# Kernel tuning notes

Hardware: AMD Instinct MI355X
Metric: run time of the kernel (lower is better)

## Reference

```python
import jax, jax.numpy as jnp
import numpy as np

H, N, CH = 256, 64, 1

def _r2c(x):
    return x[..., 0] + 1j * x[..., 1]

def setup_inputs() -> dict:
    key = jax.random.key(0)
    kA, kB, kC, kdt = jax.random.split(key, 4)
    # Build a Hurwitz A (skew-Hermitian - 0.5*I) so dA = (I-dt/2 A)^-1 (I+dt/2 A) has spectral radius < 1
    M = jax.random.normal(kA, (H, N, N, 2), dtype=jnp.float32) / np.float32(np.sqrt(N))
    Mc = _r2c(M)
    Ac = 0.5 * (Mc - jnp.conjugate(jnp.swapaxes(Mc, -1, -2))) - 0.5 * jnp.eye(N, dtype=Mc.dtype)
    A = jnp.stack([Ac.real, Ac.imag], axis=-1)  # (H,N,N,2)
    B = jax.random.normal(kB, (H, N, 2), dtype=jnp.float32)
    C = jax.random.normal(kC, (CH, H, N, 2), dtype=jnp.float32)
    # log_dt uniform in [log(1e-3), log(1e-1)], shape (H,1) per bilinear docstring
    log_dt = jax.random.uniform(kdt, (H, 1), dtype=jnp.float32,
                                minval=np.float32(np.log(1e-3)), maxval=np.float32(np.log(1e-1)))
    return {"A": A, "B": B, "C": C, "log_dt": log_dt, "L": 2048}

def _bilinear(dt, Ac, Bc):
    # dt: (H,1), Ac: (H,N,N) complex, Bc: (H,N) complex
    n = Ac.shape[-1]
    I = jnp.eye(n, dtype=Ac.dtype)
    half = (dt.astype(Ac.real.dtype) / 2)[:, None]  # (H,1,1)
    A_back = I - half * Ac
    A_fwd = I + half * Ac
    dB = dt.astype(Ac.dtype) * jnp.linalg.solve(A_back, Bc[..., None])[..., 0]  # (H,N)
    dA = jnp.linalg.solve(A_back, A_fwd)  # (H,N,N)
    return dA, dB

def _krylov(L, dA, dB):
    # x[..., l] = dA^l dB via squaring-doubling, matches S4 krylov math
    x = dB[..., None]  # (H,N,1)
    A_ = dA
    while x.shape[-1] < L:
        x = jnp.concatenate([x, jnp.einsum('hnm,hml->hnl', A_, x)], axis=-1)
        A_ = A_ @ A_
    return x[..., :L]

def reference(A, B, C, log_dt, L):
    Ac, Bc, Cc = _r2c(A), _r2c(B), _r2c(C)
    dt = jnp.exp(log_dt)  # (H,1)
    dA, dB = _bilinear(dt, Ac, Bc)
    x = _krylov(L, dA, dB)  # (H,N,L) complex
    # k[c,h,l] = sum_n C[c,h,n] * (dA^l dB)[h,n]; torch .float() on complex keeps real part
    k = jnp.einsum('chn,hnl->chl', Cc, x).real.astype(jnp.float32)
    return k
```

## Files before the change

kernel.cpp:

```cpp
#include <hip/hip_runtime.h>
#include <math.h>

#define NH   256
#define NN   64
#define LSEQ 2048
#define RSW  68
#define NTH  1024

typedef __attribute__((ext_vector_type(8))) short short8;
typedef __attribute__((ext_vector_type(4))) float float4_t;
typedef __attribute__((ext_vector_type(16))) float float16_t;
typedef unsigned short u16;

#define MFMA(a,b,c)   __builtin_amdgcn_mfma_f32_16x16x32_bf16((a),(b),(c),0,0,0)
#define MFMA32(a,b,c) __builtin_amdgcn_mfma_f32_32x32x16_bf16((a),(b),(c),0,0,0)
#define PERM_HI 0x07060302u
#define PERM_LO 0x05040100u

static __device__ __forceinline__ void split2(float v, unsigned& hb, unsigned& lb) {
    hb = __float_as_uint(v) & 0xffff0000u;
    lb = __float_as_uint(v - __uint_as_float(hb));
}
static __device__ __forceinline__ unsigned pack2(float v) {
    unsigned hb, lb; split2(v, hb, lb);
    return __builtin_amdgcn_perm(hb, lb, PERM_HI);
}
static __device__ __forceinline__ float unpack2(unsigned w) {
    return __uint_as_float(w & 0xffff0000u) + __uint_as_float(w << 16);
}
static __device__ __forceinline__ short8 neg8(short8 v) {
    union { short8 s; int i[4]; } u; u.s = v;
#pragma unroll
    for (int m = 0; m < 4; ++m) u.i[m] ^= 0x80008000;
    return u.s;
}

static __device__ __forceinline__ void frag_packed(const unsigned* p, short8& hi, short8& lo) {
    const uint4* q = (const uint4*)p;
    uint4 d0 = q[0], d1 = q[1];
    unsigned e[8] = {d0.x, d0.y, d0.z, d0.w, d1.x, d1.y, d1.z, d1.w};
    union { short8 s; unsigned u[4]; } H, L;
#pragma unroll
    for (int m = 0; m < 4; ++m) {
        H.u[m] = __builtin_amdgcn_perm(e[2*m+1], e[2*m], PERM_HI);
        L.u[m] = __builtin_amdgcn_perm(e[2*m+1], e[2*m], PERM_LO);
    }
    hi = H.s; lo = L.s;
}

static __device__ __forceinline__ void frag_vals(const unsigned* e, short8& hi, short8& lo) {
    unsigned lb[8];
#pragma unroll
    for (int m = 0; m < 8; ++m) {
        unsigned hv = e[m] & 0xffff0000u;
        lb[m] = __float_as_uint(__uint_as_float(e[m]) - __uint_as_float(hv));
    }
    union { short8 s; unsigned u[4]; } H, L;
#pragma unroll
    for (int m = 0; m < 4; ++m) {
        H.u[m] = __builtin_amdgcn_perm(e[2*m+1],  e[2*m],  PERM_HI);
        L.u[m] = __builtin_amdgcn_perm(lb[2*m+1], lb[2*m], PERM_HI);
    }
    hi = H.s; lo = L.s;
}


template<bool IMAG>
static __device__ __forceinline__ void cmm_pp(
    const unsigned* __restrict__ Aprl, const unsigned* __restrict__ ApiI,
    const unsigned* __restrict__ Bprl, const unsigned* __restrict__ BpiI,
    int arow, int bcol, int fq,
    float4_t& accP, float4_t& accN, float4_t& accI1, float4_t& accI2)
{
#pragma unroll
    for (int ks = 0; ks < 2; ++ks) {
        const int k0 = ks*32 + fq*8;
        short8 Arh, Arl, Aih, Ail, Brh, Brl, Bih, Bil;
        frag_packed(Aprl + arow*RSW + k0, Arh, Arl);
        frag_packed(ApiI + arow*RSW + k0, Aih, Ail);
        frag_packed(Bprl + bcol*RSW + k0, Brh, Brl);
        frag_packed(BpiI + bcol*RSW + k0, Bih, Bil);
        accP = MFMA(Arh, Brh, accP); accP = MFMA(Arh, Brl, accP); accP = MFMA(Arl, Brh, accP);
        accN = MFMA(Aih, Bih, accN); accN = MFMA(Aih, Bil, accN); accN = MFMA(Ail, Bih, accN);
        if (IMAG) {
            accI1 = MFMA(Arh, Bih, accI1); accI1 = MFMA(Arh, Bil, accI1); accI1 = MFMA(Arl, Bih, accI1);
            accI2 = MFMA(Aih, Brh, accI2); accI2 = MFMA(Aih, Brl, accI2); accI2 = MFMA(Ail, Brh, accI2);
        }
    }
}

static __device__ __forceinline__ void cmm_pair_pp(
    const unsigned* __restrict__ Aprl, const unsigned* __restrict__ ApiI,
    const unsigned* __restrict__ Bprl, const unsigned* __restrict__ BpiI,
    int arow, int bcol0, int fq,
    float4_t& P0, float4_t& N0, float4_t& I10, float4_t& I20,
    float4_t& P1, float4_t& N1, float4_t& I11, float4_t& I21)
{
#pragma unroll
    for (int ks = 0; ks < 2; ++ks) {
        const int k0 = ks*32 + fq*8;
        short8 Arh, Arl, Aih, Ail;
        frag_packed(Aprl + arow*RSW + k0, Arh, Arl);
        frag_packed(ApiI + arow*RSW + k0, Aih, Ail);
#pragma unroll
        for (int p = 0; p < 2; ++p) {
            short8 Brh, Brl, Bih, Bil;
            frag_packed(Bprl + (bcol0 + p*16)*RSW + k0, Brh, Brl);
            frag_packed(BpiI + (bcol0 + p*16)*RSW + k0, Bih, Bil);
            float4_t &aP = p ? P1 : P0, &aN = p ? N1 : N0;
            float4_t &aI1 = p ? I11 : I10, &aI2 = p ? I21 : I20;
            aP = MFMA(Arh, Brh, aP); aP = MFMA(Arh, Brl, aP); aP = MFMA(Arl, Brh, aP);
            aN = MFMA(Aih, Bih, aN); aN = MFMA(Aih, Bil, aN); aN = MFMA(Ail, Bih, aN);
            aI1 = MFMA(Arh, Bih, aI1); aI1 = MFMA(Arh, Bil, aI1); aI1 = MFMA(Arl, Bih, aI1);
            aI2 = MFMA(Aih, Brh, aI2); aI2 = MFMA(Aih, Brl, aI2); aI2 = MFMA(Ail, Brh, aI2);
        }
    }
}

static __device__ __forceinline__ void cmm32_pp(
    const unsigned* __restrict__ Aprl, const unsigned* __restrict__ ApiI,
    const unsigned* __restrict__ Bprl, const unsigned* __restrict__ BpiI,
    int arow, int bcol, int khalf,
    float16_t& R, float16_t& I)
{
#pragma unroll
    for (int ks = 0; ks < 4; ++ks) {
        const int k0 = ks*16 + khalf;
        short8 Arh, Arl, Aih, Ail, Brh, Brl, Bih, Bil;
        frag_packed(Aprl + arow*RSW + k0, Arh, Arl);
        frag_packed(ApiI + arow*RSW + k0, Aih, Ail);
        frag_packed(Bprl + bcol*RSW + k0, Brh, Brl);
        frag_packed(BpiI + bcol*RSW + k0, Bih, Bil);
        short8 nAih = neg8(Aih), nAil = neg8(Ail);
        R = MFMA32(Arh, Brh, R);  I = MFMA32(Arh, Bih, I);
        R = MFMA32(Arh, Brl, R);  I = MFMA32(Arh, Bil, I);
        R = MFMA32(Arl, Brh, R);  I = MFMA32(Arl, Bih, I);
        R = MFMA32(nAih, Bih, R); I = MFMA32(Aih, Brh, I);
        R = MFMA32(nAih, Bil, R); I = MFMA32(Ail, Brh, I);
        R = MFMA32(nAil, Bih, R); I = MFMA32(Aih, Brl, I);
    }
}

static __device__ __forceinline__ void store_XTp(
    unsigned* XTrl, unsigned* XTiI, int rowbase, int col,
    const float* p_r, const float* p_i)
{
    uint4 w;
    w.x = pack2(p_r[0]); w.y = pack2(p_r[1]); w.z = pack2(p_r[2]); w.w = pack2(p_r[3]);
    *(uint4*)&XTrl[col*RSW + rowbase] = w;
    w.x = pack2(p_i[0]); w.y = pack2(p_i[1]); w.z = pack2(p_i[2]); w.w = pack2(p_i[3]);
    *(uint4*)&XTiI[col*RSW + rowbase] = w;
}

__global__ __launch_bounds__(NTH, 4) void ssm_kernel(
    const float* __restrict__ Ag,
    const float* __restrict__ Bg,
    const float* __restrict__ Cg,
    const float* __restrict__ LogDt,
    float* __restrict__ outp)
{
    __shared__ __align__(16) unsigned char lds[157696];
    unsigned* XRrl  = (unsigned*)(lds);
    unsigned* XRiI  = (unsigned*)(lds + 17408);
    unsigned* XT0rl = (unsigned*)(lds + 34816);
    unsigned* XT0iI = (unsigned*)(lds + 52224);
    unsigned* XT1rl = (unsigned*)(lds + 69632);
    unsigned* XT1iI = (unsigned*)(lds + 87040);
    unsigned* XFrl  = (unsigned*)(lds + 104448);
    unsigned* XFiI  = (unsigned*)(lds + 121856);
    unsigned* Gmrl  = (unsigned*)(lds + 139264);
    unsigned* GmiI  = (unsigned*)(lds + 147968);
    float* bvr = (float*)(lds + 156672);
    float* bvi = (float*)(lds + 156928);
    float* urr = (float*)(lds + 157184);
    float* uri = (float*)(lds + 157440);

    const int t    = threadIdx.x;
    const int lane = t & 63;
    const int wv   = t >> 6;
    const int fm   = lane & 15, fq = lane >> 4;
    const int h    = blockIdx.x;

    const int tip  = wv >> 1, tjp = wv & 1;
    const int parow = tip*16 + fm;
    const int pb0   = tjp*32 + fm;

    const int ti2 = (wv >> 1) & 1, tj2 = wv & 1;
    const int arow32 = ti2*32 + (lane & 31);
    const int bcol32 = tj2*32 + (lane & 31);
    const int khalf  = (lane >> 5) * 8;

    const float dt  = expf(LogDt[h]);
    const float hdt = 0.5f * dt;

    const float2* A2 = (const float2*)(Ag + (size_t)h * NN * NN * 2);
    const float4_t z4 = {0.f, 0.f, 0.f, 0.f};

#pragma unroll
    for (int e = 0; e < 4; ++e) {
        int idx = t + e*NTH;
        int i = idx >> 6, j = idx & 63;
        float2 a = A2[idx];
        float x1r = (i == j ? 1.0f : 0.0f) + hdt * a.x;
        float x1i = hdt * a.y;
        unsigned wr = pack2(x1r), wi = pack2(x1i);
        XRrl[i*RSW + j] = wr;
        XRiI[i*RSW + j] = wi;
        XT0rl[j*RSW + i] = wr;
        XT0iI[j*RSW + i] = wi;
    }
    if (t < NN) {
        float2 bv = ((const float2*)Bg)[h*NN + t];
        float2 cv = ((const float2*)Cg)[h*NN + t];
        bvr[t] = bv.x; bvi[t] = bv.y;
        Gmrl[t] = pack2(cv.x);
        GmiI[t] = pack2(cv.y);
    }
    __syncthreads();

    if (wv < 8) {
        float4_t P0 = z4, N0 = z4, I10 = z4, I20 = z4;
        float4_t P1 = z4, N1 = z4, I11 = z4, I21 = z4;
#pragma unroll
        for (int ks = 0; ks < 2; ++ks) {
            const int k0 = ks*32 + fq*8;
            unsigned vr[8], vi[8];
#pragma unroll
            for (int j = 0; j < 8; ++j) {
                float2 a = A2[parow*NN + k0 + j];
                vr[j] = __float_as_uint((parow == k0 + j ? 1.0f : 0.0f) - hdt * a.x);
                vi[j] = __float_as_uint(-hdt * a.y);
            }
            short8 Arh, Arl, Aih, Ail;
            frag_vals(vr, Arh, Arl);
            frag_vals(vi, Aih, Ail);
#pragma unroll
            for (int p = 0; p < 2; ++p) {
                short8 Brh, Brl, Bih, Bil;
                frag_packed(XT0rl + (pb0 + p*16)*RSW + k0, Brh, Brl);
                frag_packed(XT0iI + (pb0 + p*16)*RSW + k0, Bih, Bil);
                float4_t &aP = p ? P1 : P0, &aN = p ? N1 : N0;
                float4_t &aI1 = p ? I11 : I10, &aI2 = p ? I21 : I20;
                aP = MFMA(Arh, Brh, aP); aP = MFMA(Arh, Brl, aP); aP = MFMA(Arl, Brh, aP);
                aN = MFMA(Aih, Bih, aN); aN = MFMA(Aih, Bil, aN); aN = MFMA(Ail, Bih, aN);
                aI1 = MFMA(Arh, Bih, aI1); aI1 = MFMA(Arh, Bil, aI1); aI1 = MFMA(Arl, Bih, aI1);
                aI2 = MFMA(Aih, Brh, aI2); aI2 = MFMA(Aih, Brl, aI2); aI2 = MFMA(Ail, Brh, aI2);
            }
        }
#pragma unroll
        for (int p = 0; p < 2; ++p) {
            const int bcol = pb0 + p*16;
            const float4_t &aP = p ? P1 : P0, &aN = p ? N1 : N0;
            const float4_t &aI1 = p ? I11 : I10, &aI2 = p ? I21 : I20;
#pragma unroll
            for (int rp = 0; rp < 2; ++rp) {
                int row0 = tip*16 + fq*4 + rp*2;
                uint2 w;
                w.x = pack2(aP[rp*2]   - aN[rp*2]);
                w.y = pack2(aP[rp*2+1] - aN[rp*2+1]);
                *(uint2*)&XFrl[bcol*RSW + row0] = w;
                w.x = pack2(aI1[rp*2]   + aI2[rp*2]);
                w.y = pack2(aI1[rp*2+1] + aI2[rp*2+1]);
                *(uint2*)&XFiI[bcol*RSW + row0] = w;
            }
        }
    }
    __syncthreads();

    {
        float4_t P0 = z4, N0 = z4, I10 = z4, I20 = z4;
        float4_t P1 = z4, N1 = z4, I11 = z4, I21 = z4;
        if (wv < 8)
            cmm_pair_pp(XRrl, XRiI, XFrl, XFiI, parow, pb0, fq, P0, N0, I10, I20, P1, N1, I11, I21);
        __syncthreads();
        if (wv < 8) {
#pragma unroll
            for (int p = 0; p < 2; ++p) {
                const int bcol = pb0 + p*16;
#pragma unroll
                for (int r = 0; r < 4; ++r) {
                    int row = tip*16 + fq*4 + r;
                    float vr = (p ? P1[r] : P0[r]) - (p ? N1[r] : N0[r]);
                    float vi = (p ? I11[r] : I10[r]) + (p ? I21[r] : I20[r]);
                    XRrl[row*RSW + bcol] = pack2(vr);
                    XRiI[row*RSW + bcol] = pack2(vi);
                }
            }
        }
    }
    __syncthreads();

    {
        float p_r[2][4], p_i[2][4];
        if (wv < 8) {
            float4_t P0 = z4, N0 = z4, I10 = z4, I20 = z4;
            float4_t P1 = z4, N1 = z4, I11 = z4, I21 = z4;
            cmm_pair_pp(XRrl, XRiI, XFrl, XFiI, parow, pb0, fq, P0, N0, I10, I20, P1, N1, I11, I21);
#pragma unroll
            for (int p = 0; p < 2; ++p) {
                const int bcol = pb0 + p*16;
                const float4_t &aP = p ? P1 : P0, &aN = p ? N1 : N0;
                const float4_t &aI1 = p ? I11 : I10, &aI2 = p ? I21 : I20;
#pragma unroll
                for (int r = 0; r < 4; ++r) {
                    int row = tip*16 + fq*4 + r;
                    float2 a = A2[row*NN + bcol];
                    float dd  = (row == bcol ? 1.0f : 0.0f);
                    float x1r = dd + hdt * a.x;
                    float x1i = hdt * a.y;
                    float vvr = unpack2(XRrl[row*RSW + bcol]);
                    float vvi = unpack2(XRiI[row*RSW + bcol]);
                    p_r[p][r] = 2.0f*(3.0f*x1r - 3.0f*vvr + (aP[r] - aN[r])) - dd;
                    p_i[p][r] = 2.0f*(3.0f*x1i - 3.0f*vvi + (aI1[r] + aI2[r]));
                }
                store_XTp(XT0rl, XT0iI, tip*16 + fq*4, bcol, p_r[p], p_i[p]);
            }
        }
        __syncthreads();
        if (wv < 8) {
#pragma unroll
            for (int p = 0; p < 2; ++p) {
                const int bcol = pb0 + p*16;
#pragma unroll
                for (int r = 0; r < 4; ++r) {
                    int row = tip*16 + fq*4 + r;
                    XRrl[row*RSW + bcol] = pack2(p_r[p][r]);
                    XRiI[row*RSW + bcol] = pack2(p_i[p][r]);
                }
            }
        }
    }
    __syncthreads();

    {
        int n = t >> 4, part = t & 15;
        uint4 Wr = *(const uint4*)(XRrl + n*RSW + part*4);
        uint4 Wi = *(const uint4*)(XRiI + n*RSW + part*4);
        unsigned wr[4] = {Wr.x, Wr.y, Wr.z, Wr.w};
        unsigned wi[4] = {Wi.x, Wi.y, Wi.z, Wi.w};
        float ar = 0.f, ai = 0.f;
#pragma unroll
        for (int e = 0; e < 4; ++e) {
            float mr = unpack2(wr[e]);
            float mi = unpack2(wi[e]);
            int k = part*4 + e;
            ar += mr*bvr[k] - mi*bvi[k];
            ai += mr*bvi[k] + mi*bvr[k];
        }
#pragma unroll
        for (int off = 8; off; off >>= 1) { ar += __shfl_xor(ar, off); ai += __shfl_xor(ai, off); }
        if (part == 0) { urr[n] = ar; uri[n] = ai; }
    }
    __syncthreads();

#pragma unroll 1
    for (int s = 1; s <= 9; ++s) {
        unsigned* XTcrl = (s & 1) ? XT0rl : XT1rl;
        unsigned* XTciI = (s & 1) ? XT0iI : XT1iI;
        unsigned* XTnrl = (s & 1) ? XT1rl : XT0rl;
        unsigned* XTniI = (s & 1) ? XT1iI : XT0iI;
        float16_t sR, sI;
        if (wv >= 8) {
            if (s == 1) {
                int n = (t >> 3) & 63, part = t & 7;
                const unsigned* rp0 = XRrl + n*RSW + part*8;
                const unsigned* ip0 = XRiI + n*RSW + part*8;
                uint4 Wr0 = *(const uint4*)(rp0), Wr1 = *(const uint4*)(rp0 + 4);
                uint4 Wi0 = *(const uint4*)(ip0), Wi1 = *(const uint4*)(ip0 + 4);
                unsigned wr[8] = {Wr0.x, Wr0.y, Wr0.z, Wr0.w, Wr1.x, Wr1.y, Wr1.z, Wr1.w};
                unsigned wi[8] = {Wi0.x, Wi0.y, Wi0.z, Wi0.w, Wi1.x, Wi1.y, Wi1.z, Wi1.w};
                float ar = 0.f, ai = 0.f;
#pragma unroll
                for (int e = 0; e < 8; ++e) {
                    float mr = unpack2(wr[e]);
                    float mi = unpack2(wi[e]);
                    int k = part*8 + e;
                    ar += mr*urr[k] - mi*uri[k];
                    ai += mr*uri[k] + mi*urr[k];
                }
#pragma unroll
                for (int off = 4; off; off >>= 1) { ar += __shfl_xor(ar, off); ai += __shfl_xor(ai, off); }
                if (part == 0) {
                    float u_r = urr[n], u_i = uri[n];
                    XFrl[n]       = pack2(hdt*(u_r + bvr[n]));
                    XFiI[n]       = pack2(hdt*(u_i + bvi[n]));
                    XFrl[RSW + n] = pack2(hdt*(ar + u_r));
                    XFiI[RSW + n] = pack2(hdt*(ai + u_i));
                }
            } else if (s <= 6) {
                const int C = 1 << (s-1);
                const int w = wv - 8;
                const int nT = (s == 6) ? 8 : 4;
                if (w < nT) {
                    const int rt = w >> 2, ct = w & 3;
                    float4_t aP = z4, aN = z4, aI1 = z4, aI2 = z4;
                    cmm_pp<true>(XFrl, XFiI, XRrl, XRiI, rt*16 + fm, ct*16 + fm, fq, aP, aN, aI1, aI2);
#pragma unroll
                    for (int r = 0; r < 4; ++r) {
                        int orow = C + rt*16 + fq*4 + r;
                        int oc   = ct*16 + fm;
                        XFrl[orow*RSW + oc] = pack2(aP[r] - aN[r]);
                        XFiI[orow*RSW + oc] = pack2(aI1[r] + aI2[r]);
                    }
                }
            } else {
                const int C = 1 << (s-7);
                const int w = wv - 8;
                if (w < 4) {
                    float4_t aP = z4, aN = z4, aI1 = z4, aI2 = z4;
                    cmm_pp<true>(Gmrl, GmiI, XTcrl, XTciI, fm, w*16 + fm, fq, aP, aN, aI1, aI2);
#pragma unroll
                    for (int r = 0; r < 4; ++r) {
                        int orow = C + fq*4 + r;
                        int oc   = w*16 + fm;
                        Gmrl[orow*RSW + oc] = pack2(aP[r] - aN[r]);
                        GmiI[orow*RSW + oc] = pack2(aI1[r] + aI2[r]);
                    }
                }
            }
        } else if (wv < 4) {
#pragma unroll
            for (int g = 0; g < 16; ++g) { sR[g] = 0.f; sI[g] = 0.f; }
            __builtin_amdgcn_s_setprio(1);
            cmm32_pp(XRrl, XRiI, XTcrl, XTciI, arow32, bcol32, khalf, sR, sI);
            __builtin_amdgcn_s_setprio(0);
            {
                const int col = tj2*32 + (lane & 31);
                const int hi4 = (lane >> 5) * 4;
#pragma unroll
                for (int q = 0; q < 4; ++q) {
                    float r4[4], i4[4];
#pragma unroll
                    for (int rr = 0; rr < 4; ++rr) { r4[rr] = sR[4*q+rr]; i4[rr] = sI[4*q+rr]; }
                    store_XTp(XTnrl, XTniI, ti2*32 + 8*q + hi4, col, r4, i4);
                }
            }
        }
        __syncthreads();
        if (wv < 4 && s < 9) {
            const int col = tj2*32 + (lane & 31);
            const int hi4 = (lane >> 5) * 4;
#pragma unroll
            for (int q = 0; q < 4; ++q) {
                const int rowb = ti2*32 + 8*q + hi4;
#pragma unroll
                for (int rr = 0; rr < 4; ++rr) {
                    XRrl[(rowb + rr)*RSW + col] = pack2(sR[4*q+rr]);
                    XRiI[(rowb + rr)*RSW + col] = pack2(sI[4*q+rr]);
                }
            }
        }
        __syncthreads();
    }

#pragma unroll 1
    for (int tt = 0; tt < 4; ++tt) {
        if (tt < 3 && wv < 4) {
            const int ab = tt * 8;
            float4_t aP = z4, aN = z4, aI1 = z4, aI2 = z4;
            cmm_pp<true>(Gmrl, GmiI, XT1rl, XT1iI, ab + fm, wv*16 + fm, fq, aP, aN, aI1, aI2);
#pragma unroll
            for (int r = 0; r < 4; ++r) {
                int orow = 8 + ab + fq*4 + r;
                if (orow < 32) {
                    int oc = wv*16 + fm;
                    Gmrl[orow*RSW + oc] = pack2(aP[r] - aN[r]);
                    GmiI[orow*RSW + oc] = pack2(aI1[r] + aI2[r]);
                }
            }
        }
        if (wv >= 4 && wv < 8) {
            const int jb = tt * 8;
            int ga = jb + fm; if (ga > 31) ga = 31;
            float4_t aP = z4, aN = z4, aI1 = z4, aI2 = z4;
            __builtin_amdgcn_s_setprio(1);
            cmm_pp<false>(Gmrl, GmiI, XFrl, XFiI, ga, (wv-4)*16 + fm, fq, aP, aN, aI1, aI2);
            __builtin_amdgcn_s_setprio(0);
            if (fq < 2) {
                size_t base = (size_t)h * LSEQ;
#pragma unroll
                for (int r = 0; r < 4; ++r)
                    outp[base + (jb + fq*4 + r)*NN + (wv-4)*16 + fm] = aP[r] - aN[r];
            }
        }
        if (tt < 3) __syncthreads();
    }
}

extern "C" void kernel_launch(void* const* d_in, const int* in_sizes, int n_in,
                              void* d_out, int out_size, void* d_ws, size_t ws_size,
                              hipStream_t stream) {
    const float* A  = (const float*)d_in[0];
    const float* B  = (const float*)d_in[1];
    const float* C  = (const float*)d_in[2];
    const float* ld = (const float*)d_in[3];
    float* out = (float*)d_out;
    ssm_kernel<<<dim3(NH), dim3(NTH), 0, stream>>>(A, B, C, ld, out);
}
```

Baseline: 91.86 us.

## Overlap dB matvec prep on idle waves and drop a serial matvec stage

The matrix-vector products that build the seed vector u (A·B, Y·B, and the two products with the current matrix) now run on the otherwise idle waves 8-15 while waves 0-7 do the MFMA matrix steps. u is reassembled algebraically from those pieces, so the separate block-wide matvec phase and its barrier are removed. The final loop barrier is also skipped on the last iteration. This trades extra LDS scratch and a different floating-point evaluation order for fewer serialized phases and barriers.

```diff
diff --git a/kernel.cpp b/kernel.cpp
--- a/kernel.cpp
+++ b/kernel.cpp
@@ -159,7 +159,7 @@
     const float* __restrict__ LogDt,
     float* __restrict__ outp)
 {
-    __shared__ __align__(16) unsigned char lds[157696];
+    __shared__ __align__(16) unsigned char lds[159232];
     unsigned* XRrl  = (unsigned*)(lds);
     unsigned* XRiI  = (unsigned*)(lds + 17408);
     unsigned* XT0rl = (unsigned*)(lds + 34816);
@@ -172,8 +172,14 @@
     unsigned* GmiI  = (unsigned*)(lds + 147968);
     float* bvr = (float*)(lds + 156672);
     float* bvi = (float*)(lds + 156928);
-    float* urr = (float*)(lds + 157184);
-    float* uri = (float*)(lds + 157440);
+    float* abr = (float*)(lds + 157184);
+    float* abi = (float*)(lds + 157440);
+    float* w1r = (float*)(lds + 157696);
+    float* w1i = (float*)(lds + 157952);
+    float* vbr = (float*)(lds + 158208);
+    float* vbi = (float*)(lds + 158464);
+    float* vwr = (float*)(lds + 158720);
+    float* vwi = (float*)(lds + 158976);
 
     const int t    = threadIdx.x;
     const int lane = t & 63;
@@ -264,14 +270,42 @@
                 *(uint2*)&XFiI[bcol*RSW + row0] = w;
             }
         }
+    } else {
+        int n = (t >> 3) & 63, part = t & 7;
+        float ar = 0.f, ai = 0.f;
+#pragma unroll
+        for (int e = 0; e < 8; ++e) {
+            int k = part*8 + e;
+            float2 a = A2[n*NN + k];
+            ar += a.x*bvr[k] - a.y*bvi[k];
+            ai += a.x*bvi[k] + a.y*bvr[k];
+        }
+#pragma unroll
+        for (int off = 4; off; off >>= 1) { ar += __shfl_xor(ar, off); ai += __shfl_xor(ai, off); }
+        if (part == 0) { abr[n] = ar; abi[n] = ai; }
     }
     __syncthreads();
 
     {
         float4_t P0 = z4, N0 = z4, I10 = z4, I20 = z4;
         float4_t P1 = z4, N1 = z4, I11 = z4, I21 = z4;
-        if (wv < 8)
+        if (wv < 8) {
             cmm_pair_pp(XRrl, XRiI, XFrl, XFiI, parow, pb0, fq, P0, N0, I10, I20, P1, N1, I11, I21);
+        } else {
+            int i = (t >> 3) & 63, part = t & 7;
+            float wr_ = 0.f, wi_ = 0.f;
+#pragma unroll
+            for (int e = 0; e < 8; ++e) {
+                int j = part*8 + e;
+                float yr = unpack2(XFrl[j*RSW + i]);
+                float yi = unpack2(XFiI[j*RSW + i]);
+                wr_ += yr*bvr[j] - yi*bvi[j];
+                wi_ += yr*bvi[j] + yi*bvr[j];
+            }
+#pragma unroll
+            for (int off = 4; off; off >>= 1) { wr_ += __shfl_xor(wr_, off); wi_ += __shfl_xor(wi_, off); }
+            if (part == 0) { w1r[i] = wr_; w1i[i] = wi_; }
+        }
         __syncthreads();
         if (wv < 8) {
 #pragma unroll
@@ -315,6 +349,31 @@
                 }
                 store_XTp(XT0rl, XT0iI, tip*16 + fq*4, bcol, p_r[p], p_i[p]);
             }
+        } else {
+            int n = (t >> 3) & 63, part = t & 7;
+            const unsigned* rp0 = XRrl + n*RSW + part*8;
+            const unsigned* ip0 = XRiI + n*RSW + part*8;
+            uint4 Wr0 = *(const uint4*)(rp0), Wr1 = *(const uint4*)(rp0 + 4);
+            uint4 Wi0 = *(const uint4*)(ip0), Wi1 = *(const uint4*)(ip0 + 4);
+            unsigned wrr[8] = {Wr0.x, Wr0.y, Wr0.z, Wr0.w, Wr1.x, Wr1.y, Wr1.z, Wr1.w};
+            unsigned wii[8] = {Wi0.x, Wi0.y, Wi0.z, Wi0.w, Wi1.x, Wi1.y, Wi1.z, Wi1.w};
+            float br_ = 0.f, bi_ = 0.f, wr_ = 0.f, wi_ = 0.f;
+#pragma unroll
+            for (int e = 0; e < 8; ++e) {
+                int k = part*8 + e;
+                float mr = unpack2(wrr[e]);
+                float mi = unpack2(wii[e]);
+                br_ += mr*bvr[k] - mi*bvi[k];
+                bi_ += mr*bvi[k] + mi*bvr[k];
+                wr_ += mr*w1r[k] - mi*w1i[k];
+                wi_ += mr*w1i[k] + mi*w1r[k];
+            }
+#pragma unroll
+            for (int off = 4; off; off >>= 1) {
+                br_ += __shfl_xor(br_, off); bi_ += __shfl_xor(bi_, off);
+                wr_ += __shfl_xor(wr_, off); wi_ += __shfl_xor(wi_, off);
+            }
+            if (part == 0) { vbr[n] = br_; vbi[n] = bi_; vwr[n] = wr_; vwi[n] = wi_; }
         }
         __syncthreads();
         if (wv < 8) {
@@ -329,27 +388,6 @@
                 }
             }
         }
-    }
-    __syncthreads();
-
-    {
-        int n = t >> 4, part = t & 15;
-        uint4 Wr = *(const uint4*)(XRrl + n*RSW + part*4);
-        uint4 Wi = *(const uint4*)(XRiI + n*RSW + part*4);
-        unsigned wr[4] = {Wr.x, Wr.y, Wr.z, Wr.w};
-        unsigned wi[4] = {Wi.x, Wi.y, Wi.z, Wi.w};
-        float ar = 0.f, ai = 0.f;
-#pragma unroll
-        for (int e = 0; e < 4; ++e) {
-            float mr = unpack2(wr[e]);
-            float mi = unpack2(wi[e]);
-            int k = part*4 + e;
-            ar += mr*bvr[k] - mi*bvi[k];
-            ai += mr*bvi[k] + mi*bvr[k];
-        }
-#pragma unroll
-        for (int off = 8; off; off >>= 1) { ar += __shfl_xor(ar, off); ai += __shfl_xor(ai, off); }
-        if (part == 0) { urr[n] = ar; uri[n] = ai; }
     }
     __syncthreads();
 
@@ -367,25 +405,43 @@
                 const unsigned* ip0 = XRiI + n*RSW + part*8;
                 uint4 Wr0 = *(const uint4*)(rp0), Wr1 = *(const uint4*)(rp0 + 4);
                 uint4 Wi0 = *(const uint4*)(ip0), Wi1 = *(const uint4*)(ip0 + 4);
-                unsigned wr[8] = {Wr0.x, Wr0.y, Wr0.z, Wr0.w, Wr1.x, Wr1.y, Wr1.z, Wr1.w};
-                unsigned wi[8] = {Wi0.x, Wi0.y, Wi0.z, Wi0.w, Wi1.x, Wi1.y, Wi1.z, Wi1.w};
+                unsigned wrr[8] = {Wr0.x, Wr0.y, Wr0.z, Wr0.w, Wr1.x, Wr1.y, Wr1.z, Wr1.w};
+                unsigned wii[8] = {Wi0.x, Wi0.y, Wi0.z, Wi0.w, Wi1.x, Wi1.y, Wi1.z, Wi1.w};
+                const int kb = part*8;
+                float4_t b4r0 = *(const float4_t*)&bvr[kb], b4r1 = *(const float4_t*)&bvr[kb+4];
+                float4_t b4i0 = *(const float4_t*)&bvi[kb], b4i1 = *(const float4_t*)&bvi[kb+4];
+                float4_t a4r0 = *(const float4_t*)&abr[kb], a4r1 = *(const float4_t*)&abr[kb+4];
+                float4_t a4i0 = *(const float4_t*)&abi[kb], a4i1 = *(const float4_t*)&abi[kb+4];
+                float4_t v4r0 = *(const float4_t*)&vbr[kb], v4r1 = *(const float4_t*)&vbr[kb+4];
+                float4_t v4i0 = *(const float4_t*)&vbi[kb], v4i1 = *(const float4_t*)&vbi[kb+4];
+                float4_t w4r0 = *(const float4_t*)&vwr[kb], w4r1 = *(const float4_t*)&vwr[kb+4];
+                float4_t w4i0 = *(const float4_t*)&vwi[kb], w4i1 = *(const float4_t*)&vwi[kb+4];
+                const float c6h = 6.0f * hdt;
                 float ar = 0.f, ai = 0.f;
 #pragma unroll
                 for (int e = 0; e < 8; ++e) {
-                    float mr = unpack2(wr[e]);
-                    float mi = unpack2(wi[e]);
-                    int k = part*8 + e;
-                    ar += mr*urr[k] - mi*uri[k];
-                    ai += mr*uri[k] + mi*urr[k];
+                    float bkr = (e < 4) ? b4r0[e] : b4r1[e-4];
+                    float bki = (e < 4) ? b4i0[e] : b4i1[e-4];
+                    float ur = 5.0f*bkr + c6h*((e < 4) ? a4r0[e] : a4r1[e-4])
+                             - 6.0f*((e < 4) ? v4r0[e] : v4r1[e-4])
+                             + 2.0f*((e < 4) ? w4r0[e] : w4r1[e-4]);
+                    float ui = 5.0f*bki + c6h*((e < 4) ? a4i0[e] : a4i1[e-4])
+                             - 6.0f*((e < 4) ? v4i0[e] : v4i1[e-4])
+                             + 2.0f*((e < 4) ? w4i0[e] : w4i1[e-4]);
+                    float mr = unpack2(wrr[e]);
+                    float mi = unpack2(wii[e]);
+                    ar += mr*ur - mi*ui;
+                    ai += mr*ui + mi*ur;
                 }
 #pragma unroll
                 for (int off = 4; off; off >>= 1) { ar += __shfl_xor(ar, off); ai += __shfl_xor(ai, off); }
                 if (part == 0) {
-                    float u_r = urr[n], u_i = uri[n];
-                    XFrl[n]       = pack2(hdt*(u_r + bvr[n]));
-                    XFiI[n]       = pack2(hdt*(u_i + bvi[n]));
-                    XFrl[RSW + n] = pack2(hdt*(ar + u_r));
-                    XFiI[RSW + n] = pack2(hdt*(ai + u_i));
+                    float un_r = 5.0f*bvr[n] + c6h*abr[n] - 6.0f*vbr[n] + 2.0f*vwr[n];
+                    float un_i = 5.0f*bvi[n] + c6h*abi[n] - 6.0f*vbi[n] + 2.0f*vwi[n];
+                    XFrl[n]       = pack2(hdt*(un_r + bvr[n]));
+                    XFiI[n]       = pack2(hdt*(un_i + bvi[n]));
+                    XFrl[RSW + n] = pack2(hdt*(ar + un_r));
+                    XFiI[RSW + n] = pack2(hdt*(ai + un_i));
                 }
             } else if (s <= 6) {
                 const int C = 1 << (s-1);
@@ -450,7 +506,7 @@
                 }
             }
         }
-        __syncthreads();
+        if (s < 9) __syncthreads();
     }
 
 #pragma unroll 1
```

After: 106.0 us. 1.15x slower.
